# Kernel tuning notes

Hardware: AMD Instinct MI355X
Metric: run time of the kernel (lower is better)

The kernel has to match this reference:

```python
import jax, jax.numpy as jnp
import numpy as np

N_NODES = 50000
N_EDGES = 800000
D = 64
E_DIM = 2
C = 8


def _spline_basis(pseudo, K):
    """Open B-spline basis, degree=1. pseudo: [Ne, E] in [0,1).
    Returns basis B [Ne, S] and flat weight index WI [Ne, S], S = 2**E."""
    E = pseudo.shape[1]
    v = pseudo * (K - 1)
    lo_f = jnp.floor(v)
    frac = v - lo_f
    lo = lo_f.astype(jnp.int32)
    idx = jnp.stack([jnp.clip(lo, 0, K - 1), jnp.clip(lo + 1, 0, K - 1)], axis=-1)  # [Ne,E,2]
    bas = jnp.stack([1.0 - frac, frac], axis=-1)                                   # [Ne,E,2]
    combos = jnp.asarray(
        np.stack(np.meshgrid(*([np.arange(2)] * E), indexing='ij'), -1).reshape(-1, E)
    )  # [S,E]
    d_idx = jnp.arange(E)[None, :]          # broadcast to [S,E]
    B = jnp.prod(bas[:, d_idx, combos], axis=-1)  # [Ne,S]
    stride = (K ** jnp.arange(E)).astype(jnp.int32)  # [E]
    WI = jnp.sum(idx[:, d_idx, combos] * stride[None, None, :], axis=-1)  # [Ne,S]
    return B, WI


def _spline_conv(x, src, dst, pseudo, W, root, bias, K, num_nodes):
    """SplineConv (degree=1, open spline, aggr='mean', root_weight, bias).
    x: [N,Din], W: [K**E, Din, Dout], root: [Din, Dout]."""
    B, WI = _spline_basis(pseudo, K)                 # [Ne,S], [Ne,S]
    Y = jnp.einsum('nd,kdo->nko', x, W)              # [N, K**E, Dout]
    gathered = Y[src[:, None], WI]                   # [Ne, S, Dout]
    m = jnp.einsum('es,eso->eo', B, gathered)        # [Ne, Dout]
    msum = jax.ops.segment_sum(m, dst, num_segments=num_nodes)
    cnt = jax.ops.segment_sum(jnp.ones((m.shape[0], 1), m.dtype), dst, num_segments=num_nodes)
    aggr = msum / jnp.maximum(cnt, 1.0)
    return aggr + x @ root + bias


def setup_inputs() -> dict:
    key = jax.random.key(0)
    ks = jax.random.split(key, 16)
    s = 1.0 / np.sqrt(D)
    return {
        'x': jax.random.normal(ks[0], (N_NODES, D), jnp.float32),
        'edge_index': jax.random.randint(ks[1], (2, N_EDGES), 0, N_NODES, jnp.int32),
        'edge_attr': jax.random.uniform(ks[2], (N_EDGES, E_DIM), jnp.float32),
        'W1': jax.random.normal(ks[3], (3 ** E_DIM, D, D), jnp.float32) * s,
        'root1': jax.random.normal(ks[4], (D, D), jnp.float32) * s,
        'b1': jax.random.normal(ks[5], (D,), jnp.float32) * 0.01,
        'W2': jax.random.normal(ks[6], (5 ** E_DIM, D, D), jnp.float32) * s,
        'root2': jax.random.normal(ks[7], (D, D), jnp.float32) * s,
        'b2': jax.random.normal(ks[8], (D,), jnp.float32) * 0.01,
        'mlp1_w': jax.random.normal(ks[9], (D, D), jnp.float32) * s,
        'mlp1_b': jax.random.normal(ks[10], (D,), jnp.float32) * 0.01,
        'mlp2_w': jax.random.normal(ks[11], (D, C), jnp.float32) * s,
        'mlp2_b': jax.random.normal(ks[12], (C,), jnp.float32) * 0.01,
    }


def reference(x, edge_index, edge_attr, W1, root1, b1, W2, root2, b2,
              mlp1_w, mlp1_b, mlp2_w, mlp2_b):
    N = x.shape[0]
    src, dst = edge_index[0], edge_index[1]
    h = jax.nn.elu(_spline_conv(x, src, dst, edge_attr, W1, root1, b1, 3, N))
    # dropout is identity in eval mode
    h = jax.nn.elu(_spline_conv(h, src, dst, edge_attr, W2, root2, b2, 5, N))
    # task='node', G=0 -> no pooling / no concat
    h = jax.nn.relu(h @ mlp1_w + mlp1_b)
    h = jax.nn.relu(h @ mlp2_w + mlp2_b)
    return h
```

## Files before the change

kernel.cpp:

```cpp
#include <hip/hip_runtime.h>
#include <hip/hip_bf16.h>

typedef __attribute__((ext_vector_type(8))) short short8;
typedef __attribute__((ext_vector_type(4))) float floatx4;
typedef __attribute__((ext_vector_type(16))) float floatx16;

__device__ __forceinline__ unsigned short f2bf(float x) {
  __hip_bfloat16 h = __float2bfloat16(x);
  return __builtin_bit_cast(unsigned short, h);
}
__device__ __forceinline__ float bf2f(unsigned short u) {
  return __builtin_bit_cast(float, (unsigned int)u << 16);
}

__global__ __launch_bounds__(256) void cvt_x_kernel(
    const float* __restrict__ X, unsigned short* __restrict__ Xbf, int n) {
  int i = blockIdx.x * 256 + threadIdx.x;
  if (i < n) Xbf[i] = f2bf(X[i]);
}

__global__ __launch_bounds__(256) void pack_b_kernel(
    const float* __restrict__ W, const float* __restrict__ root,
    unsigned short* __restrict__ Bpk, int K2) {
  int R = (K2 + 1) * 64;
  int total = 64 * R;
  int i = blockIdx.x * 256 + threadIdx.x;
  if (i >= total) return;
  int j = i & 7;
  int lane = (i >> 3) & 63;
  int rest = i >> 9;
  int wv = rest & 3, kc = rest >> 2;
  int o = wv * 16 + (lane & 15);
  int p = kc * 32 + ((lane >> 4) & 3) * 8 + j;
  int k = p >> 6, q6 = p & 63;
  int d = (k < K2) ? (((q6 & 1) << 5) | (q6 >> 1)) : q6;
  float v = (k < K2) ? W[(k << 12) + (d << 6) + o] : root[(d << 6) + o];
  Bpk[i] = f2bf(v);
}

__global__ __launch_bounds__(256) void zero_int_kernel(int* __restrict__ p, int n) {
  int i = blockIdx.x * 256 + threadIdx.x;
  if (i < n) p[i] = 0;
}

__global__ __launch_bounds__(256) void hist_kernel(
    const int* __restrict__ dst, int* __restrict__ deg, int nE) {
  int e = blockIdx.x * 256 + threadIdx.x;
  if (e < nE) atomicAdd(&deg[dst[e]], 1);
}

__global__ __launch_bounds__(256) void blocksum_kernel(
    const int* __restrict__ deg, int* __restrict__ partial, int N) {
  __shared__ int s[256];
  int t = threadIdx.x, i = blockIdx.x * 256 + t;
  s[t] = (i < N) ? deg[i] : 0;
  __syncthreads();
  for (int off = 128; off > 0; off >>= 1) {
    if (t < off) s[t] += s[t + off];
    __syncthreads();
  }
  if (t == 0) partial[blockIdx.x] = s[0];
}

__global__ __launch_bounds__(256) void scanpartials_kernel(
    int* __restrict__ partial, int nb) {
  __shared__ int s[256];
  int t = threadIdx.x;
  int v = (t < nb) ? partial[t] : 0;
  s[t] = v;
  __syncthreads();
  for (int off = 1; off < 256; off <<= 1) {
    int x = (t >= off) ? s[t - off] : 0;
    __syncthreads();
    s[t] += x;
    __syncthreads();
  }
  if (t < nb) partial[t] = s[t] - v;
}

__global__ __launch_bounds__(256) void blockscan_kernel(
    const int* __restrict__ deg, const int* __restrict__ partial,
    int* __restrict__ row_start, int* __restrict__ cursor, int N, int nE) {
  __shared__ int s[256];
  int t = threadIdx.x, i = blockIdx.x * 256 + t;
  int v = (i < N) ? deg[i] : 0;
  s[t] = v;
  __syncthreads();
  for (int off = 1; off < 256; off <<= 1) {
    int x = (t >= off) ? s[t - off] : 0;
    __syncthreads();
    s[t] += x;
    __syncthreads();
  }
  if (i < N) {
    int excl = s[t] - v + partial[blockIdx.x];
    row_start[i] = excl;
    cursor[i] = excl;
  }
  if (i == 0) row_start[N] = nE;
}

__global__ __launch_bounds__(256) void scatter_rec_kernel(
    const int* __restrict__ dst, const int* __restrict__ src,
    const float* __restrict__ attr, int* __restrict__ cursor,
    float4* __restrict__ rec3, float4* __restrict__ rec5, int nE) {
  int e = blockIdx.x * 256 + threadIdx.x;
  if (e >= nE) return;
  int pos = atomicAdd(&cursor[dst[e]], 1);
  float2 a = *(const float2*)&attr[2 * e];
  float offf = __builtin_bit_cast(float, src[e] * 64);
  rec3[pos] = make_float4(a.x * 2.f, a.y * 2.f, offf, 0.f);
  rec5[pos] = make_float4(a.x * 4.f, a.y * 4.f, offf, 0.f);
}

template <int K, int K2, int OUTBF, int NODES, int GRP>
__global__ __launch_bounds__(256, 4) void spline_layer_kernel(
    const float4* __restrict__ rec, const int* __restrict__ row_start,
    const unsigned short* __restrict__ Xbf, const unsigned short* __restrict__ Bpk,
    const float* __restrict__ bias, void* __restrict__ outv, int N, int nE) {
  constexpr int RZ = K2 * 64;
  constexpr int AS = RZ + 8;
  constexpr int NKZ = RZ / 32;
  constexpr int NKC = (K2 + 1) * 2;
  constexpr int GN = NODES / 4;
  __shared__ unsigned short As[NODES * AS];
  const int t = threadIdx.x, w = t >> 6, lane = t & 63;
  const int nodeBase = blockIdx.x * NODES;

  const int col = lane & 31, half = lane >> 5;
  const float mi0f = (col < K2) ? (float)(col % K) : -1e9f;
  const float mi1f = (col < K2) ? (float)(col / K) : 0.f;

  for (int g = 0; g < GN; ++g) {
    const int row = w * GN + g;
    const int node = nodeBase + row;
    if (node < N) {
      floatx16 d0, d1;
#pragma unroll
      for (int i = 0; i < 16; ++i) { d0[i] = 0.f; d1[i] = 0.f; }

      const int beg = row_start[node], end = row_start[node + 1];
      for (int c0 = beg; c0 < end; c0 += 16) {
        const int ib = c0 + half * 8;
        float4 rj[8];
#pragma unroll
        for (int j = 0; j < 8; ++j)
          rj[j] = rec[min(ib + j, nE - 1)];
        short8 A, Blo, Bhi;
#pragma unroll
        for (int j = 0; j < 8; ++j) {
          float su = fmaxf(0.f, 1.f - fabsf(mi0f - rj[j].x));
          float sv = fmaxf(0.f, 1.f - fabsf(mi1f - rj[j].y));
          float p = (ib + j < end) ? su * sv : 0.f;
          A[j] = (short)f2bf(p);
          const unsigned short* xp =
              Xbf + __builtin_bit_cast(int, rj[j].z) + col;
          Blo[j] = (short)xp[0];
          Bhi[j] = (short)xp[32];
        }
        d0 = __builtin_amdgcn_mfma_f32_32x32x16_bf16(A, Blo, d0, 0, 0, 0);
        d1 = __builtin_amdgcn_mfma_f32_32x32x16_bf16(A, Bhi, d1, 0, 0, 0);
      }

      const float inv = 1.f / (float)max(end - beg, 1);
#pragma unroll
      for (int reg = 0; reg < 16; ++reg) {
        int r = (reg & 3) + 8 * (reg >> 2) + 4 * half;
        if (r < K2) {
          unsigned int pk =
              ((unsigned int)f2bf(d1[reg] * inv) << 16) | f2bf(d0[reg] * inv);
          *(unsigned int*)&As[row * AS + r * 64 + col * 2] = pk;
        }
      }
    } else {
      for (int i = lane; i < RZ / 2; i += 64)
        ((unsigned int*)&As[row * AS])[i] = 0;
    }
  }
  __syncthreads();

  const int mrow = lane & 15, q = lane >> 4;
  const int arow = (NODES < 16) ? min(mrow, NODES - 1) : mrow;
  const int anode = min(nodeBase + arow, N - 1);
  floatx4 acc = {0.f, 0.f, 0.f, 0.f};
#pragma unroll
  for (int kc0 = 0; kc0 < NKC; kc0 += GRP) {
    short8 av[GRP], bv[GRP];
#pragma unroll
    for (int u = 0; u < GRP; ++u) {
      const int kc = kc0 + u;
      if (kc < NKZ)
        av[u] = *(const short8*)&As[arow * AS + kc * 32 + q * 8];
      else
        av[u] = *(const short8*)&Xbf[(size_t)anode * 64 + (kc - NKZ) * 32 + q * 8];
      bv[u] = *(const short8*)&Bpk[(((size_t)kc * 4 + w) * 64 + lane) * 8];
    }
#pragma unroll
    for (int u = 0; u < GRP; ++u)
      acc = __builtin_amdgcn_mfma_f32_16x16x32_bf16(av[u], bv[u], acc, 0, 0, 0);
  }

  const int o = w * 16 + mrow;
  const float bvs = bias[o];
#pragma unroll
  for (int reg = 0; reg < 4; ++reg) {
    int rloc = q * 4 + reg;
    int node = nodeBase + rloc;
    if (rloc < NODES && node < N) {
      float v = acc[reg] + bvs;
      v = v > 0.f ? v : (expf(v) - 1.f);
      if (OUTBF)
        ((unsigned short*)outv)[(size_t)node * 64 + o] = f2bf(v);
      else
        ((float*)outv)[(size_t)node * 64 + o] = v;
    }
  }
}

__global__ __launch_bounds__(256) void head_kernel(
    const unsigned short* __restrict__ h2bf, const unsigned short* __restrict__ m1pk,
    const float* __restrict__ m1b, const float* __restrict__ m2w,
    const float* __restrict__ m2b, float* __restrict__ out, int N) {
  __shared__ unsigned short Hs[64 * 72];
  __shared__ unsigned short Ts[64 * 72];
  __shared__ float W2s[512];
  const int t = threadIdx.x, w = t >> 6, lane = t & 63;
  const int n0 = blockIdx.x * 64;

  for (int i = t; i < 512; i += 256) {
    int row = i >> 3, cg = i & 7;
    int n = n0 + row;
    floatx4 val = {0.f, 0.f, 0.f, 0.f};
    if (n < N) val = *(const floatx4*)&h2bf[(size_t)n * 64 + cg * 8];
    *(floatx4*)&Hs[row * 72 + cg * 8] = val;
  }
  for (int i = t; i < 512; i += 256) W2s[i] = m2w[i];
  __syncthreads();

  const int mrow = lane & 15, q = lane >> 4;
  const int o = w * 16 + mrow;
  const float bv = m1b[o];
#pragma unroll
  for (int rg = 0; rg < 4; ++rg) {
    floatx4 acc = {0.f, 0.f, 0.f, 0.f};
#pragma unroll
    for (int kc = 0; kc < 2; ++kc) {
      short8 a = *(const short8*)&Hs[(rg * 16 + mrow) * 72 + kc * 32 + q * 8];
      short8 b = *(const short8*)&m1pk[(((size_t)kc * 4 + w) * 64 + lane) * 8];
      acc = __builtin_amdgcn_mfma_f32_16x16x32_bf16(a, b, acc, 0, 0, 0);
    }
#pragma unroll
    for (int reg = 0; reg < 4; ++reg) {
      int row = rg * 16 + q * 4 + reg;
      float v = acc[reg] + bv;
      Ts[row * 72 + o] = f2bf(v > 0.f ? v : 0.f);
    }
  }
  __syncthreads();

  for (int i = t; i < 512; i += 256) {
    int nl = i >> 3, c = i & 7;
    int n = n0 + nl;
    if (n >= N) continue;
    float s = m2b[c];
    for (int d = 0; d < 64; ++d) s += bf2f(Ts[nl * 72 + d]) * W2s[d * 8 + c];
    out[(size_t)n * 8 + c] = s > 0.f ? s : 0.f;
  }
}

extern "C" void kernel_launch(void* const* d_in, const int* in_sizes, int n_in,
                              void* d_out, int out_size, void* d_ws, size_t ws_size,
                              hipStream_t stream) {
  const float* x     = (const float*)d_in[0];
  const int*   ei    = (const int*)d_in[1];
  const float* attr  = (const float*)d_in[2];
  const float* W1    = (const float*)d_in[3];
  const float* root1 = (const float*)d_in[4];
  const float* b1    = (const float*)d_in[5];
  const float* W2    = (const float*)d_in[6];
  const float* root2 = (const float*)d_in[7];
  const float* b2    = (const float*)d_in[8];
  const float* m1w   = (const float*)d_in[9];
  const float* m1b   = (const float*)d_in[10];
  const float* m2w   = (const float*)d_in[11];
  const float* m2b   = (const float*)d_in[12];

  const int N  = in_sizes[0] / 64;
  const int nE = in_sizes[1] / 2;
  const int* src  = ei;
  const int* dstv = ei + nE;
  float* out = (float*)d_out;

  int* deg       = (int*)d_ws;
  int* row_start = deg + N;
  int* cursor    = row_start + (N + 1);
  int* partial   = cursor + N;
  char* pbase = (char*)(partial + 256);
  pbase = (char*)(((uintptr_t)pbase + 15) & ~(uintptr_t)15);
  float4* rec3 = (float4*)pbase;
  float4* rec5 = rec3 + nE;
  unsigned short* Xbf  = (unsigned short*)(rec5 + nE);
  unsigned short* h1bf = Xbf + (size_t)N * 64;
  unsigned short* h2bf = h1bf + (size_t)N * 64;
  unsigned short* Bpk1 = h2bf + (size_t)N * 64;
  unsigned short* Bpk2 = Bpk1 + 64 * 640;
  unsigned short* m1pk = Bpk2 + 64 * 1664;

  dim3 blk(256);
  int nbN  = (N + 255) / 256;
  int nbE  = (nE + 255) / 256;
  int nbF1 = (N + 15) / 16;
  int nbF2 = (N + 11) / 12;
  int nbH  = (N + 63) / 64;

  zero_int_kernel<<<nbN, blk, 0, stream>>>(deg, N);
  hist_kernel<<<nbE, blk, 0, stream>>>(dstv, deg, nE);
  blocksum_kernel<<<nbN, blk, 0, stream>>>(deg, partial, N);
  scanpartials_kernel<<<1, blk, 0, stream>>>(partial, nbN);
  blockscan_kernel<<<nbN, blk, 0, stream>>>(deg, partial, row_start, cursor, N, nE);
  scatter_rec_kernel<<<nbE, blk, 0, stream>>>(dstv, src, attr, cursor, rec3, rec5, nE);

  pack_b_kernel<<<(64 * 640 + 255) / 256, blk, 0, stream>>>(W1, root1, Bpk1, 9);
  pack_b_kernel<<<(64 * 1664 + 255) / 256, blk, 0, stream>>>(W2, root2, Bpk2, 25);
  pack_b_kernel<<<(64 * 64 + 255) / 256, blk, 0, stream>>>(m1w, m1w, m1pk, 0);
  cvt_x_kernel<<<(N * 64 + 255) / 256, blk, 0, stream>>>(x, Xbf, N * 64);

  spline_layer_kernel<3, 9, 1, 16, 2><<<nbF1, blk, 0, stream>>>(
      rec3, row_start, Xbf, Bpk1, b1, h1bf, N, nE);

  spline_layer_kernel<5, 25, 1, 12, 4><<<nbF2, blk, 0, stream>>>(
      rec5, row_start, h1bf, Bpk2, b2, h2bf, N, nE);

  head_kernel<<<nbH, blk, 0, stream>>>(h2bf, m1pk, m1b, m2w, m2b, out, N);
}
```

Baseline: 319.2 us.

## Share one edge record buffer, vectorize X gathers, defer mean scaling to epilogue

Replaces the two per-layer edge record arrays with a single one scaled for K=5, with a runtime uscale factor for K=3. A 16-entry zero pad removes the clamp on record loads. Each lane now loads X features as one 32-bit pair and splits it with perm, instead of two strided 16-bit loads, and the pack layout changes to match. The 1/deg mean scaling moves from the bf16 aggregation store to the fp32 epilogue, with separate accumulators for the spline and root parts. Other changes: cvt_x is vectorized, layer 1 uses a different GRP, and launch bounds change. The result is less scatter write traffic and fewer gather instructions, at the cost of more accumulator registers and a changed bf16 rounding point.

```diff
diff --git a/kernel.cpp b/kernel.cpp
--- a/kernel.cpp
+++ b/kernel.cpp
@@ -2,6 +2,8 @@
 #include <hip/hip_bf16.h>
 
 typedef __attribute__((ext_vector_type(8))) short short8;
+typedef __attribute__((ext_vector_type(4))) short short4v;
+typedef __attribute__((ext_vector_type(4))) unsigned int uint4v;
 typedef __attribute__((ext_vector_type(4))) float floatx4;
 typedef __attribute__((ext_vector_type(16))) float floatx16;
 
@@ -12,11 +14,19 @@
 __device__ __forceinline__ float bf2f(unsigned short u) {
   return __builtin_bit_cast(float, (unsigned int)u << 16);
 }
+__device__ __forceinline__ unsigned int pk_bf16(float lo, float hi) {
+  return ((unsigned int)f2bf(hi) << 16) | (unsigned int)f2bf(lo);
+}
 
 __global__ __launch_bounds__(256) void cvt_x_kernel(
-    const float* __restrict__ X, unsigned short* __restrict__ Xbf, int n) {
+    const float4* __restrict__ X, unsigned short* __restrict__ Xbf, int n4) {
   int i = blockIdx.x * 256 + threadIdx.x;
-  if (i < n) Xbf[i] = f2bf(X[i]);
+  if (i < n4) {
+    float4 v = X[i];
+    short4v o = {(short)f2bf(v.x), (short)f2bf(v.y),
+                 (short)f2bf(v.z), (short)f2bf(v.w)};
+    *(short4v*)&Xbf[i * 4] = o;
+  }
 }
 
 __global__ __launch_bounds__(256) void pack_b_kernel(
@@ -33,8 +43,7 @@
   int o = wv * 16 + (lane & 15);
   int p = kc * 32 + ((lane >> 4) & 3) * 8 + j;
   int k = p >> 6, q6 = p & 63;
-  int d = (k < K2) ? (((q6 & 1) << 5) | (q6 >> 1)) : q6;
-  float v = (k < K2) ? W[(k << 12) + (d << 6) + o] : root[(d << 6) + o];
+  float v = (k < K2) ? W[(k << 12) + (q6 << 6) + o] : root[(q6 << 6) + o];
   Bpk[i] = f2bf(v);
 }
 
@@ -103,33 +112,38 @@
 __global__ __launch_bounds__(256) void scatter_rec_kernel(
     const int* __restrict__ dst, const int* __restrict__ src,
     const float* __restrict__ attr, int* __restrict__ cursor,
-    float4* __restrict__ rec3, float4* __restrict__ rec5, int nE) {
+    float4* __restrict__ recS, int nE) {
   int e = blockIdx.x * 256 + threadIdx.x;
+  if (e < 16) recS[nE + e] = make_float4(0.f, 0.f, 0.f, 0.f);
   if (e >= nE) return;
   int pos = atomicAdd(&cursor[dst[e]], 1);
   float2 a = *(const float2*)&attr[2 * e];
-  float offf = __builtin_bit_cast(float, src[e] * 64);
-  rec3[pos] = make_float4(a.x * 2.f, a.y * 2.f, offf, 0.f);
-  rec5[pos] = make_float4(a.x * 4.f, a.y * 4.f, offf, 0.f);
-}
-
-template <int K, int K2, int OUTBF, int NODES, int GRP>
-__global__ __launch_bounds__(256, 4) void spline_layer_kernel(
+  recS[pos] = make_float4(a.x * 4.f, a.y * 4.f,
+                          __builtin_bit_cast(float, src[e] * 64), 0.f);
+}
+
+template <int K, int K2, int OUTBF, int NODES, int GRP, int MINW>
+__global__ __launch_bounds__(256, MINW) void spline_layer_kernel(
     const float4* __restrict__ rec, const int* __restrict__ row_start,
     const unsigned short* __restrict__ Xbf, const unsigned short* __restrict__ Bpk,
-    const float* __restrict__ bias, void* __restrict__ outv, int N, int nE) {
+    const float* __restrict__ bias, void* __restrict__ outv, int N, float uscale) {
   constexpr int RZ = K2 * 64;
   constexpr int AS = RZ + 8;
   constexpr int NKZ = RZ / 32;
   constexpr int NKC = (K2 + 1) * 2;
   constexpr int GN = NODES / 4;
   __shared__ unsigned short As[NODES * AS];
+  __shared__ __align__(16) float invs[16];
   const int t = threadIdx.x, w = t >> 6, lane = t & 63;
   const int nodeBase = blockIdx.x * NODES;
 
-  const int col = lane & 31, half = lane >> 5;
+  const int col = lane & 31, half = lane >> 5, col2 = col * 2;
   const float mi0f = (col < K2) ? (float)(col % K) : -1e9f;
   const float mi1f = (col < K2) ? (float)(col / K) : 0.f;
+
+  if constexpr (NODES < 16) {
+    if (w == 3 && lane >= 60) invs[lane - 48] = 1.0f;
+  }
 
   for (int g = 0; g < GN; ++g) {
     const int row = w * GN + g;
@@ -140,39 +154,47 @@
       for (int i = 0; i < 16; ++i) { d0[i] = 0.f; d1[i] = 0.f; }
 
       const int beg = row_start[node], end = row_start[node + 1];
+      if (lane == 0) invs[row] = 1.f / (float)max(end - beg, 1);
       for (int c0 = beg; c0 < end; c0 += 16) {
         const int ib = c0 + half * 8;
+        const int rem = end - ib;
         float4 rj[8];
 #pragma unroll
-        for (int j = 0; j < 8; ++j)
-          rj[j] = rec[min(ib + j, nE - 1)];
-        short8 A, Blo, Bhi;
+        for (int j = 0; j < 8; ++j) rj[j] = rec[ib + j];
+        short8 A;
+        unsigned int xv[8];
 #pragma unroll
         for (int j = 0; j < 8; ++j) {
-          float su = fmaxf(0.f, 1.f - fabsf(mi0f - rj[j].x));
-          float sv = fmaxf(0.f, 1.f - fabsf(mi1f - rj[j].y));
-          float p = (ib + j < end) ? su * sv : 0.f;
+          float t0 = fmaf(rj[j].x, -uscale, mi0f);
+          float t1 = fmaf(rj[j].y, -uscale, mi1f);
+          float su = fmaxf(0.f, 1.f - fabsf(t0));
+          float sv = fmaxf(0.f, 1.f - fabsf(t1));
+          float p = (j < rem) ? su * sv : 0.f;
           A[j] = (short)f2bf(p);
-          const unsigned short* xp =
-              Xbf + __builtin_bit_cast(int, rj[j].z) + col;
-          Blo[j] = (short)xp[0];
-          Bhi[j] = (short)xp[32];
+          xv[j] = *(const unsigned int*)(Xbf +
+                    (__builtin_bit_cast(int, rj[j].z) + col2));
         }
-        d0 = __builtin_amdgcn_mfma_f32_32x32x16_bf16(A, Blo, d0, 0, 0, 0);
-        d1 = __builtin_amdgcn_mfma_f32_32x32x16_bf16(A, Bhi, d1, 0, 0, 0);
+        uint4v blo, bhi;
+#pragma unroll
+        for (int i = 0; i < 4; ++i) {
+          blo[i] = __builtin_amdgcn_perm(xv[2 * i + 1], xv[2 * i], 0x05040100u);
+          bhi[i] = __builtin_amdgcn_perm(xv[2 * i + 1], xv[2 * i], 0x07060302u);
+        }
+        d0 = __builtin_amdgcn_mfma_f32_32x32x16_bf16(
+                 A, __builtin_bit_cast(short8, blo), d0, 0, 0, 0);
+        d1 = __builtin_amdgcn_mfma_f32_32x32x16_bf16(
+                 A, __builtin_bit_cast(short8, bhi), d1, 0, 0, 0);
       }
 
-      const float inv = 1.f / (float)max(end - beg, 1);
 #pragma unroll
       for (int reg = 0; reg < 16; ++reg) {
         int r = (reg & 3) + 8 * (reg >> 2) + 4 * half;
-        if (r < K2) {
-          unsigned int pk =
-              ((unsigned int)f2bf(d1[reg] * inv) << 16) | f2bf(d0[reg] * inv);
-          *(unsigned int*)&As[row * AS + r * 64 + col * 2] = pk;
-        }
+        if (r < K2)
+          *(unsigned int*)&As[row * AS + r * 64 + col2] =
+              pk_bf16(d0[reg], d1[reg]);
       }
     } else {
+      if (lane == 0) invs[row] = 1.0f;
       for (int i = lane; i < RZ / 2; i += 64)
         ((unsigned int*)&As[row * AS])[i] = 0;
     }
@@ -182,7 +204,9 @@
   const int mrow = lane & 15, q = lane >> 4;
   const int arow = (NODES < 16) ? min(mrow, NODES - 1) : mrow;
   const int anode = min(nodeBase + arow, N - 1);
-  floatx4 acc = {0.f, 0.f, 0.f, 0.f};
+  floatx4 aZ0 = {0.f, 0.f, 0.f, 0.f};
+  floatx4 aZ1 = {0.f, 0.f, 0.f, 0.f};
+  floatx4 aR  = {0.f, 0.f, 0.f, 0.f};
 #pragma unroll
   for (int kc0 = 0; kc0 < NKC; kc0 += GRP) {
     short8 av[GRP], bv[GRP];
@@ -196,18 +220,26 @@
       bv[u] = *(const short8*)&Bpk[(((size_t)kc * 4 + w) * 64 + lane) * 8];
     }
 #pragma unroll
-    for (int u = 0; u < GRP; ++u)
-      acc = __builtin_amdgcn_mfma_f32_16x16x32_bf16(av[u], bv[u], acc, 0, 0, 0);
+    for (int u = 0; u < GRP; ++u) {
+      const int kc = kc0 + u;
+      if (kc >= NKZ)
+        aR = __builtin_amdgcn_mfma_f32_16x16x32_bf16(av[u], bv[u], aR, 0, 0, 0);
+      else if ((kc0 / GRP) & 1)
+        aZ1 = __builtin_amdgcn_mfma_f32_16x16x32_bf16(av[u], bv[u], aZ1, 0, 0, 0);
+      else
+        aZ0 = __builtin_amdgcn_mfma_f32_16x16x32_bf16(av[u], bv[u], aZ0, 0, 0, 0);
+    }
   }
 
   const int o = w * 16 + mrow;
   const float bvs = bias[o];
+  const floatx4 invv = *(const floatx4*)&invs[q * 4];
 #pragma unroll
   for (int reg = 0; reg < 4; ++reg) {
     int rloc = q * 4 + reg;
     int node = nodeBase + rloc;
     if (rloc < NODES && node < N) {
-      float v = acc[reg] + bvs;
+      float v = (aZ0[reg] + aZ1[reg]) * invv[reg] + aR[reg] + bvs;
       v = v > 0.f ? v : (expf(v) - 1.f);
       if (OUTBF)
         ((unsigned short*)outv)[(size_t)node * 64 + o] = f2bf(v);
@@ -297,9 +329,8 @@
   int* partial   = cursor + N;
   char* pbase = (char*)(partial + 256);
   pbase = (char*)(((uintptr_t)pbase + 15) & ~(uintptr_t)15);
-  float4* rec3 = (float4*)pbase;
-  float4* rec5 = rec3 + nE;
-  unsigned short* Xbf  = (unsigned short*)(rec5 + nE);
+  float4* recS = (float4*)pbase;
+  unsigned short* Xbf  = (unsigned short*)(recS + nE + 16);
   unsigned short* h1bf = Xbf + (size_t)N * 64;
   unsigned short* h2bf = h1bf + (size_t)N * 64;
   unsigned short* Bpk1 = h2bf + (size_t)N * 64;
@@ -318,18 +349,19 @@
   blocksum_kernel<<<nbN, blk, 0, stream>>>(deg, partial, N);
   scanpartials_kernel<<<1, blk, 0, stream>>>(partial, nbN);
   blockscan_kernel<<<nbN, blk, 0, stream>>>(deg, partial, row_start, cursor, N, nE);
-  scatter_rec_kernel<<<nbE, blk, 0, stream>>>(dstv, src, attr, cursor, rec3, rec5, nE);
+  scatter_rec_kernel<<<nbE, blk, 0, stream>>>(dstv, src, attr, cursor, recS, nE);
 
   pack_b_kernel<<<(64 * 640 + 255) / 256, blk, 0, stream>>>(W1, root1, Bpk1, 9);
   pack_b_kernel<<<(64 * 1664 + 255) / 256, blk, 0, stream>>>(W2, root2, Bpk2, 25);
   pack_b_kernel<<<(64 * 64 + 255) / 256, blk, 0, stream>>>(m1w, m1w, m1pk, 0);
-  cvt_x_kernel<<<(N * 64 + 255) / 256, blk, 0, stream>>>(x, Xbf, N * 64);
-
-  spline_layer_kernel<3, 9, 1, 16, 2><<<nbF1, blk, 0, stream>>>(
-      rec3, row_start, Xbf, Bpk1, b1, h1bf, N, nE);
-
-  spline_layer_kernel<5, 25, 1, 12, 4><<<nbF2, blk, 0, stream>>>(
-      rec5, row_start, h1bf, Bpk2, b2, h2bf, N, nE);
+  cvt_x_kernel<<<(N * 16 + 255) / 256, blk, 0, stream>>>(
+      (const float4*)x, Xbf, N * 16);
+
+  spline_layer_kernel<3, 9, 1, 16, 4, 6><<<nbF1, blk, 0, stream>>>(
+      recS, row_start, Xbf, Bpk1, b1, h1bf, N, 0.5f);
+
+  spline_layer_kernel<5, 25, 1, 12, 4, 4><<<nbF2, blk, 0, stream>>>(
+      recS, row_start, h1bf, Bpk2, b2, h2bf, N, 1.0f);
 
   head_kernel<<<nbH, blk, 0, stream>>>(h2bf, m1pk, m1b, m2w, m2b, out, N);
 }
```

After: 315.0 us. Within noise of the previous version (-1.3%).
